# Kernel tuning notes

Measured on AMD Instinct MI355X. Metric: run time of the kernel, lower is better.

The kernel has to match this reference:

```python
import jax, jax.numpy as jnp
import numpy as np

EPS = 1e-08

def squash(x, axis=-1):
    sq = jnp.sum(x * x, axis=axis, keepdims=True)
    scale = sq / (1.0 + sq)
    return scale * x / jnp.sqrt(sq + EPS)

def setup_inputs() -> dict:
    key = jax.random.key(0)
    k1, _ = jax.random.split(key)
    B, IC, OC, D = 128, 1152, 10, 16
    u_predict = jax.random.normal(k1, (B, IC, OC, D), dtype=jnp.float32)
    b = jnp.zeros((IC, OC), dtype=jnp.float32)  # nn.Parameter init
    return {"u_predict": u_predict, "b": b}

def reference(u_predict, b, n_iterations: int = 3):
    # u_predict: (B, IC, OC, D); b: (IC, OC)
    c = jax.nn.softmax(b, axis=1)[None, :, :, None]        # (1, IC, OC, 1)
    s = jnp.sum(c * u_predict, axis=1)                      # (B, OC, D)
    v = squash(s, axis=-1)
    if n_iterations <= 0:
        return v
    b_batch = jnp.broadcast_to(b, u_predict.shape[:3])      # (B, IC, OC)
    for _ in range(n_iterations):
        # agreement: <u_hat, v> over output_dim
        b_batch = b_batch + jnp.einsum('bijd,bjd->bij', u_predict, v)
        c = jax.nn.softmax(b_batch, axis=2)[..., None]      # (B, IC, OC, 1)
        s = jnp.sum(c * u_predict, axis=1)                  # (B, OC, D)
        v = squash(s, axis=-1)
    return v
```

## Files before the change

kernel.cpp:

```cpp
#include <hip/hip_runtime.h>
#include <hip/hip_bf16.h>


#define B_     128
#define IC_    1152
#define OC_    10
#define ROW_   160
#define WPS_   80
#define PARTS_ 8
#define SPB_   144
#define UPB_   9
#define SOUT_  20480

typedef float v2f __attribute__((ext_vector_type(2)));

__device__ __forceinline__ float bf_lo(uint32_t w) { return __uint_as_float(w << 16); }
__device__ __forceinline__ float bf_hi(uint32_t w) { return __uint_as_float(w & 0xffff0000u); }

template<int CTRL>
__device__ __forceinline__ float dppf(float x) {
    return __int_as_float(__builtin_amdgcn_update_dpp(
        0, __float_as_int(x), CTRL, 0xF, 0xF, true));
}
__device__ __forceinline__ float dpp_sum8(float x) {
    x += dppf<0xB1>(x);
    x += dppf<0x4E>(x);
    x += dppf<0x141>(x);
    return x;
}
__device__ __forceinline__ float softmax10(float own[5]) {
    float m = own[0];
#pragma unroll
    for (int k = 1; k < 5; ++k) m = fmaxf(m, own[k]);
    m = fmaxf(m, dppf<0x128>(m));
    float sum = 0.f;
#pragma unroll
    for (int k = 0; k < 5; ++k) { own[k] = __expf(own[k] - m); sum += own[k]; }
    sum += dppf<0x128>(sum);
    return 1.f / sum;
}
__device__ __forceinline__ float squash_row(float x) {
    float sq = x * x;
    sq += __shfl_xor(sq, 1, 16);
    sq += __shfl_xor(sq, 2, 16);
    sq += __shfl_xor(sq, 4, 16);
    sq += __shfl_xor(sq, 8, 16);
    return (sq / (1.f + sq)) * x * rsqrtf(sq + 1e-8f);
}

__global__ __launch_bounds__(256) void a_kernel(
    const float* __restrict__ u, const float* __restrict__ b_in,
    uint32_t* __restrict__ u16, float* __restrict__ s0_part,
    float* __restrict__ s_red)
{
    const int bid = blockIdx.x, tid = threadIdx.x;
    const int l = tid & 15, h = l >> 3, g = tid >> 4;
    const int b = bid >> 3, part = bid & 7;
    const int wave = tid >> 6, lane = tid & 63;

    const int gidx = bid * 256 + tid;
    if (gidx < 3 * SOUT_) s_red[gidx] = 0.f;

    __shared__ float red[4][ROW_];
    __shared__ float b_lds[SPB_ * OC_];

#pragma unroll
    for (int it = 0; it < 6; ++it) {
        int idx = it * 256 + tid;
        if (idx < SPB_ * OC_) b_lds[idx] = b_in[part * SPB_ * OC_ + idx];
    }
    __syncthreads();

    float2 sc[5];
#pragma unroll
    for (int k = 0; k < 5; ++k) { sc[k].x = 0.f; sc[k].y = 0.f; }
#pragma unroll
    for (int uu = 0; uu < UPB_; ++uu) {
        const int su = uu * 16 + g;
        const int i  = part * SPB_ + su;
        const v2f* up = (const v2f*)(u + (size_t)(b * IC_ + i) * ROW_ + 2 * l);
        v2f uv[5];
#pragma unroll
        for (int k = 0; k < 5; ++k) uv[k] = __builtin_nontemporal_load(up + 16 * k);

        uint32_t* wp = u16 + (size_t)(b * IC_ + i) * WPS_;
#pragma unroll
        for (int k = 0; k < 5; ++k) {
            __hip_bfloat16 bx = __float2bfloat16(uv[k].x);
            __hip_bfloat16 by = __float2bfloat16(uv[k].y);
            wp[16 * k + l] = ((uint32_t)(*(const uint16_t*)&by) << 16) |
                              (uint32_t)(*(const uint16_t*)&bx);
        }
        float own[5];
#pragma unroll
        for (int k = 0; k < 5; ++k) own[k] = b_lds[su * OC_ + 2 * k + h];
        const float inv = softmax10(own);
#pragma unroll
        for (int k = 0; k < 5; ++k) {
            float c = own[k] * inv;
            sc[k].x += c * uv[k].x; sc[k].y += c * uv[k].y;
        }
    }
#pragma unroll
    for (int k = 0; k < 5; ++k) {
        sc[k].x += __shfl_xor(sc[k].x, 16); sc[k].y += __shfl_xor(sc[k].y, 16);
        sc[k].x += __shfl_xor(sc[k].x, 32); sc[k].y += __shfl_xor(sc[k].y, 32);
    }
    if (lane < 16) {
#pragma unroll
        for (int k = 0; k < 5; ++k)
            *(float2*)&red[wave][32 * k + 2 * l] = sc[k];
    }
    __syncthreads();
    if (tid < ROW_) {
        float t = red[0][tid] + red[1][tid] + red[2][tid] + red[3][tid];
        s0_part[(size_t)(b * PARTS_ + part) * ROW_ + tid] = t;
    }
}

template<int T>
__global__ __launch_bounds__(256) void i_kernel(
    const uint32_t* __restrict__ u16, const float* __restrict__ b_in,
    const float* __restrict__ s0_part, const float* __restrict__ s_red_prev,
    const float* __restrict__ v_in, float* __restrict__ v_out,
    float* __restrict__ s_out)
{
    const int bid = blockIdx.x, tid = threadIdx.x;
    const int l = tid & 15, h = l >> 3, g = tid >> 4;
    const int b = bid >> 3, part = bid & 7;
    const int wave = tid >> 6, lane = tid & 63;

    __shared__ float red[4][ROW_];
    __shared__ float v_lds[ROW_];
    __shared__ float b_lds[SPB_ * OC_];

#define B_LOAD(UW, uu) do {                                                 \
        const int su_ = (uu) * 16 + g;                                      \
        const uint32_t* wp_ = u16 + (size_t)(b * IC_ + part * SPB_ + su_) * WPS_; \
        _Pragma("unroll")                                                   \
        for (int k = 0; k < 5; ++k) UW[k] = wp_[16 * k + l];                \
    } while (0)

    uint32_t uwA[5], uwB[5];
    B_LOAD(uwA, 0);
    B_LOAD(uwB, 1);

#pragma unroll
    for (int it = 0; it < 6; ++it) {
        int idx = it * 256 + tid;
        if (idx < SPB_ * OC_) b_lds[idx] = b_in[part * SPB_ * OC_ + idx];
    }

    if (tid < ROW_) {
        float vsum;
        if (T == 1) {
            const float* sp = s0_part + (size_t)(b * PARTS_) * ROW_;
            float x = 0.f;
#pragma unroll
            for (int p = 0; p < PARTS_; ++p) x += sp[p * ROW_ + tid];
            vsum = squash_row(x);
        } else {
            vsum = v_in[b * ROW_ + tid] + squash_row(s_red_prev[b * ROW_ + tid]);
        }
        if (T < 3 && part == 0) v_out[b * ROW_ + tid] = vsum;
        v_lds[tid] = vsum;
    }
    __syncthreads();

    float2 vv[5];
#pragma unroll
    for (int k = 0; k < 5; ++k)
        vv[k] = *(const float2*)&v_lds[32 * k + 2 * l];

    float2 sc[5];
#pragma unroll
    for (int k = 0; k < 5; ++k) { sc[k].x = 0.f; sc[k].y = 0.f; }

#define B_COMP(UW, uu) do {                                                 \
        const int su_ = (uu) * 16 + g;                                      \
        float own[5];                                                       \
        _Pragma("unroll")                                                   \
        for (int k = 0; k < 5; ++k) own[k] = b_lds[su_ * OC_ + 2 * k + h];  \
        _Pragma("unroll")                                                   \
        for (int k = 0; k < 5; ++k) {                                       \
            float pd = bf_lo(UW[k]) * vv[k].x + bf_hi(UW[k]) * vv[k].y;     \
            own[k] += dpp_sum8(pd);                                         \
        }                                                                   \
        const float inv = softmax10(own);                                   \
        _Pragma("unroll")                                                   \
        for (int k = 0; k < 5; ++k) {                                       \
            float c = own[k] * inv;                                         \
            sc[k].x += c * bf_lo(UW[k]); sc[k].y += c * bf_hi(UW[k]);       \
        }                                                                   \
    } while (0)

#pragma clang loop unroll(disable)
    for (int uu = 0; uu < UPB_ - 1; uu += 2) {
        B_COMP(uwA, uu);
        if (uu + 2 < UPB_) B_LOAD(uwA, uu + 2);
        B_COMP(uwB, uu + 1);
        if (uu + 3 < UPB_) B_LOAD(uwB, uu + 3);
    }
    B_COMP(uwA, UPB_ - 1);
#undef B_LOAD
#undef B_COMP

#pragma unroll
    for (int k = 0; k < 5; ++k) {
        sc[k].x += __shfl_xor(sc[k].x, 16); sc[k].y += __shfl_xor(sc[k].y, 16);
        sc[k].x += __shfl_xor(sc[k].x, 32); sc[k].y += __shfl_xor(sc[k].y, 32);
    }
    if (lane < 16) {
#pragma unroll
        for (int k = 0; k < 5; ++k)
            *(float2*)&red[wave][32 * k + 2 * l] = sc[k];
    }
    __syncthreads();
    if (tid < ROW_) {
        float t = red[0][tid] + red[1][tid] + red[2][tid] + red[3][tid];
        atomicAdd(&s_out[b * ROW_ + tid], t);
    }
}

__global__ __launch_bounds__(256) void f_kernel(
    const float* __restrict__ s3, float* __restrict__ out)
{
    const int idx = blockIdx.x * 256 + threadIdx.x;
    out[idx] = squash_row(s3[idx]);
}

extern "C" void kernel_launch(void* const* d_in, const int* in_sizes, int n_in,
                              void* d_out, int out_size, void* d_ws, size_t ws_size,
                              hipStream_t stream) {
    const float* u    = (const float*)d_in[0];
    const float* b_in = (const float*)d_in[1];
    float* out = (float*)d_out;

    float*    s0_part = (float*)d_ws;
    float*    s_red   = s0_part + (size_t)B_ * PARTS_ * ROW_;
    float*    v_acc   = s_red + 3 * SOUT_;
    uint32_t* u16     = (uint32_t*)(v_acc + 2 * SOUT_);

    const dim3 blk(256);
    const dim3 grid(B_ * PARTS_);

    a_kernel<<<grid, blk, 0, stream>>>(u, b_in, u16, s0_part, s_red);
    i_kernel<1><<<grid, blk, 0, stream>>>(u16, b_in, s0_part, nullptr,
                                          nullptr, v_acc, s_red);
    i_kernel<2><<<grid, blk, 0, stream>>>(u16, b_in, s0_part, s_red,
                                          v_acc, v_acc + SOUT_, s_red + SOUT_);
    i_kernel<3><<<grid, blk, 0, stream>>>(u16, b_in, s0_part, s_red + SOUT_,
                                          v_acc + SOUT_, nullptr, s_red + 2 * SOUT_);
    f_kernel<<<dim3(SOUT_ / 256), blk, 0, stream>>>(s_red + 2 * SOUT_, out);
}
```

Measured before the change: 68.88 us.

## Fuse final squash into last routing kernel and deepen bf16 prefetch

Removes the separate final squash kernel: the last routing iteration counts finished blocks per batch with an atomic counter and the last block applies squash and writes the output. The bf16 copy of u is repacked so each lane's five words are contiguous, and the i_kernel prefetch grows from two to four register buffers with a fully unrolled schedule. This aims to cut a launch and hide more load latency, at the cost of an extra counter, fence and sync, more registers, and a less coalesced per-lane access pattern.

```diff
diff --git a/kernel.cpp b/kernel.cpp
--- a/kernel.cpp
+++ b/kernel.cpp
@@ -47,6 +47,9 @@
     sq += __shfl_xor(sq, 8, 16);
     return (sq / (1.f + sq)) * x * rsqrtf(sq + 1e-8f);
 }
+__device__ __forceinline__ float agent_loadf(const float* p) {
+    return __hip_atomic_load(p, __ATOMIC_RELAXED, __HIP_MEMORY_SCOPE_AGENT);
+}
 
 __global__ __launch_bounds__(256) void a_kernel(
     const float* __restrict__ u, const float* __restrict__ b_in,
@@ -59,7 +62,7 @@
     const int wave = tid >> 6, lane = tid & 63;
 
     const int gidx = bid * 256 + tid;
-    if (gidx < 3 * SOUT_) s_red[gidx] = 0.f;
+    if (gidx < 3 * SOUT_ + B_) s_red[gidx] = 0.f;
 
     __shared__ float red[4][ROW_];
     __shared__ float b_lds[SPB_ * OC_];
@@ -83,13 +86,13 @@
 #pragma unroll
         for (int k = 0; k < 5; ++k) uv[k] = __builtin_nontemporal_load(up + 16 * k);
 
-        uint32_t* wp = u16 + (size_t)(b * IC_ + i) * WPS_;
+        uint32_t* wp = u16 + (size_t)(b * IC_ + i) * WPS_ + l * 5;
 #pragma unroll
         for (int k = 0; k < 5; ++k) {
             __hip_bfloat16 bx = __float2bfloat16(uv[k].x);
             __hip_bfloat16 by = __float2bfloat16(uv[k].y);
-            wp[16 * k + l] = ((uint32_t)(*(const uint16_t*)&by) << 16) |
-                              (uint32_t)(*(const uint16_t*)&bx);
+            wp[k] = ((uint32_t)(*(const uint16_t*)&by) << 16) |
+                     (uint32_t)(*(const uint16_t*)&bx);
         }
         float own[5];
 #pragma unroll
@@ -123,7 +126,8 @@
     const uint32_t* __restrict__ u16, const float* __restrict__ b_in,
     const float* __restrict__ s0_part, const float* __restrict__ s_red_prev,
     const float* __restrict__ v_in, float* __restrict__ v_out,
-    float* __restrict__ s_out)
+    float* __restrict__ s_out, uint32_t* __restrict__ cnt,
+    float* __restrict__ out)
 {
     const int bid = blockIdx.x, tid = threadIdx.x;
     const int l = tid & 15, h = l >> 3, g = tid >> 4;
@@ -134,16 +138,19 @@
     __shared__ float v_lds[ROW_];
     __shared__ float b_lds[SPB_ * OC_];
 
+    const uint32_t* ubase = u16 + (size_t)(b * IC_ + part * SPB_ + g) * WPS_ + l * 5;
+
 #define B_LOAD(UW, uu) do {                                                 \
-        const int su_ = (uu) * 16 + g;                                      \
-        const uint32_t* wp_ = u16 + (size_t)(b * IC_ + part * SPB_ + su_) * WPS_; \
-        _Pragma("unroll")                                                   \
-        for (int k = 0; k < 5; ++k) UW[k] = wp_[16 * k + l];                \
+        const uint32_t* wp_ = ubase + (size_t)(uu) * 16 * WPS_;             \
+        _Pragma("unroll")                                                   \
+        for (int k = 0; k < 5; ++k) UW[k] = wp_[k];                         \
     } while (0)
 
-    uint32_t uwA[5], uwB[5];
+    uint32_t uwA[5], uwB[5], uwC[5], uwD[5];
     B_LOAD(uwA, 0);
     B_LOAD(uwB, 1);
+    B_LOAD(uwC, 2);
+    B_LOAD(uwD, 3);
 
 #pragma unroll
     for (int it = 0; it < 6; ++it) {
@@ -194,14 +201,15 @@
         }                                                                   \
     } while (0)
 
-#pragma clang loop unroll(disable)
-    for (int uu = 0; uu < UPB_ - 1; uu += 2) {
-        B_COMP(uwA, uu);
-        if (uu + 2 < UPB_) B_LOAD(uwA, uu + 2);
-        B_COMP(uwB, uu + 1);
-        if (uu + 3 < UPB_) B_LOAD(uwB, uu + 3);
-    }
-    B_COMP(uwA, UPB_ - 1);
+    B_COMP(uwA, 0); B_LOAD(uwA, 4);
+    B_COMP(uwB, 1); B_LOAD(uwB, 5);
+    B_COMP(uwC, 2); B_LOAD(uwC, 6);
+    B_COMP(uwD, 3); B_LOAD(uwD, 7);
+    B_COMP(uwA, 4); B_LOAD(uwA, 8);
+    B_COMP(uwB, 5);
+    B_COMP(uwC, 6);
+    B_COMP(uwD, 7);
+    B_COMP(uwA, 8);
 #undef B_LOAD
 #undef B_COMP
 
@@ -220,13 +228,22 @@
         float t = red[0][tid] + red[1][tid] + red[2][tid] + red[3][tid];
         atomicAdd(&s_out[b * ROW_ + tid], t);
     }
-}
-
-__global__ __launch_bounds__(256) void f_kernel(
-    const float* __restrict__ s3, float* __restrict__ out)
-{
-    const int idx = blockIdx.x * 256 + threadIdx.x;
-    out[idx] = squash_row(s3[idx]);
+
+    if (T == 3) {
+        __shared__ int is_last;
+        __syncthreads();
+        if (tid == 0) {
+            __threadfence();
+            uint32_t old = __hip_atomic_fetch_add(&cnt[b], 1u,
+                              __ATOMIC_ACQ_REL, __HIP_MEMORY_SCOPE_AGENT);
+            is_last = (old == PARTS_ - 1);
+        }
+        __syncthreads();
+        if (is_last && tid < ROW_) {
+            float x = agent_loadf(&s_out[b * ROW_ + tid]);
+            out[b * ROW_ + tid] = squash_row(x);
+        }
+    }
 }
 
 extern "C" void kernel_launch(void* const* d_in, const int* in_sizes, int n_in,
@@ -238,7 +255,8 @@
 
     float*    s0_part = (float*)d_ws;
     float*    s_red   = s0_part + (size_t)B_ * PARTS_ * ROW_;
-    float*    v_acc   = s_red + 3 * SOUT_;
+    uint32_t* cnt     = (uint32_t*)(s_red + 3 * SOUT_);
+    float*    v_acc   = (float*)(cnt + B_);
     uint32_t* u16     = (uint32_t*)(v_acc + 2 * SOUT_);
 
     const dim3 blk(256);
@@ -246,10 +264,12 @@
 
     a_kernel<<<grid, blk, 0, stream>>>(u, b_in, u16, s0_part, s_red);
     i_kernel<1><<<grid, blk, 0, stream>>>(u16, b_in, s0_part, nullptr,
-                                          nullptr, v_acc, s_red);
+                                          nullptr, v_acc, s_red,
+                                          nullptr, nullptr);
     i_kernel<2><<<grid, blk, 0, stream>>>(u16, b_in, s0_part, s_red,
-                                          v_acc, v_acc + SOUT_, s_red + SOUT_);
+                                          v_acc, v_acc + SOUT_, s_red + SOUT_,
+                                          nullptr, nullptr);
     i_kernel<3><<<grid, blk, 0, stream>>>(u16, b_in, s0_part, s_red + SOUT_,
-                                          v_acc + SOUT_, nullptr, s_red + 2 * SOUT_);
-    f_kernel<<<dim3(SOUT_ / 256), blk, 0, stream>>>(s_red + 2 * SOUT_, out);
-}
+                                          v_acc + SOUT_, nullptr, s_red + 2 * SOUT_,
+                                          cnt, out);
+}
```

Result: slower. 103.6 us (+50.4%).
